# Performance work log

Hardware: AMD Instinct MI355X
Metric: run time of the kernel (lower is better)

The kernel has to match this reference:

```python
import jax, jax.numpy as jnp
import numpy as np

B, S, D = 2, 2048, 2048
H, NOPE, ROPE, V, C = 16, 128, 64, 128, 512
QK = NOPE + ROPE


def setup_inputs() -> dict:
    key = jax.random.key(0)
    ks = jax.random.split(key, 5)
    x = jax.random.normal(ks[0], (B, S, D), jnp.float32)
    # RoPE angle tables (seqlen, rope_dim/2)
    inv = 1.0 / (10000.0 ** (np.arange(0, ROPE, 2, dtype=np.float64) / ROPE))
    ang = np.arange(S, dtype=np.float64)[:, None] * inv[None, :]
    freqs_cos = jnp.asarray(np.cos(ang), jnp.float32)
    freqs_sin = jnp.asarray(np.sin(ang), jnp.float32)
    wq = jax.random.normal(ks[1], (H * QK, D), jnp.float32) * 0.02
    wkv_a = jax.random.normal(ks[2], (C + ROPE, D), jnp.float32) * 0.02
    wkv_b = jax.random.normal(ks[3], (H * (NOPE + V), C), jnp.float32) * 0.02
    wo = jax.random.normal(ks[4], (D, H * V), jnp.float32) * 0.02
    return {"x": x, "freqs_cos": freqs_cos, "freqs_sin": freqs_sin,
            "wq": wq, "wkv_a": wkv_a, "wkv_b": wkv_b, "wo": wo}


def _rope(t, cos, sin):
    # t: (b, s, h, r) with interleaved (real, imag) pairs, matching
    # torch.view_as_complex on reshape(..., r//2, 2)
    tr, ti = t[..., 0::2], t[..., 1::2]
    cos = cos[None, :, None, :]
    sin = sin[None, :, None, :]
    orr = tr * cos - ti * sin
    oii = tr * sin + ti * cos
    return jnp.stack([orr, oii], axis=-1).reshape(t.shape)


def _rmsnorm(t, eps=1e-6):
    return t * jax.lax.rsqrt(jnp.mean(t * t, axis=-1, keepdims=True) + eps)


def reference(x, freqs_cos, freqs_sin, wq, wkv_a, wkv_b, wo):
    # q projection (q_lora_rank == 0 -> direct)
    q = (x @ wq.T).reshape(B, S, H, QK)
    q_nope, q_pe = q[..., :NOPE], q[..., NOPE:]
    q_pe = _rope(q_pe, freqs_cos, freqs_sin)
    # latent KV compression
    kv = x @ wkv_a.T  # (b, s, C + ROPE)
    c, k_pe = kv[..., :C], kv[..., C:]
    k_pe = _rope(k_pe[:, :, None, :], freqs_cos, freqs_sin)[:, :, 0, :]  # (b, s, ROPE)
    c = _rmsnorm(c)  # cached latent (b, s, C)
    # weight absorption: wkv_b -> (H, NOPE+V, C)
    wb = wkv_b.reshape(H, NOPE + V, C)
    w_nope, w_v = wb[:, :NOPE, :], wb[:, NOPE:, :]
    q_abs = jnp.einsum('bshd,hdc->bshc', q_nope, w_nope)  # absorbed query
    scale = QK ** -0.5
    scores = (jnp.einsum('bshc,btc->bhst', q_abs, c)
              + jnp.einsum('bshr,btr->bhst', q_pe, k_pe)) * scale
    attn = jax.nn.softmax(scores, axis=-1)
    out_c = jnp.einsum('bhst,btc->bshc', attn, c)
    out = jnp.einsum('bshc,hvc->bshv', out_c, w_v)  # (b, s, h, V)
    return out.reshape(B, S, H * V) @ wo.T
```

## Files before the change

### kernel.cpp

```cpp
#include <hip/hip_runtime.h>

#define B_ 2
#define S_ 2048
#define D_ 2048
#define H_ 16
#define NOPE_ 128
#define ROPE_ 64
#define V_ 128
#define C_ 512
#define QK_ 192
#define CR_ 576
#define BS_ 4096

typedef unsigned short ushort_t;
typedef unsigned int uint_t;
typedef __attribute__((ext_vector_type(8))) short bf16x8;
typedef __attribute__((ext_vector_type(4))) float f32x4;

#define GLD16(gp, lp) __builtin_amdgcn_global_load_lds( \
    (const __attribute__((address_space(1))) void*)(gp), \
    (__attribute__((address_space(3))) void*)(lp), 16, 0, 0)

__device__ __forceinline__ float us2f(ushort_t u) {
    unsigned int x = ((unsigned int)u) << 16;
    return __uint_as_float(x);
}
__device__ __forceinline__ ushort_t f2us(float f) {
    unsigned int x = __float_as_uint(f);
    unsigned int r = (x + 0x7fffu + ((x >> 16) & 1u)) >> 16;
    return (ushort_t)r;
}

__global__ __launch_bounds__(256) void conv_all_k(
    const float* __restrict__ x,    ushort_t* __restrict__ xb,
    const float* __restrict__ wq,   ushort_t* __restrict__ wqb,
    const float* __restrict__ wo,   ushort_t* __restrict__ wob,
    const float* __restrict__ wkva, ushort_t* __restrict__ wkvab,
    const float* __restrict__ wkvb, ushort_t* __restrict__ wvb)
{
    int bid = blockIdx.x;
    if (bid < 8192) {
        long long i = ((long long)bid * 256 + threadIdx.x) * 4;
        float4 v = *reinterpret_cast<const float4*>(x + i);
        ushort4 o; o.x = f2us(v.x); o.y = f2us(v.y); o.z = f2us(v.z); o.w = f2us(v.w);
        *reinterpret_cast<ushort4*>(xb + i) = o;
    } else if (bid < 14336) {
        long long i = ((long long)(bid - 8192) * 256 + threadIdx.x) * 4;
        float4 v = *reinterpret_cast<const float4*>(wq + i);
        ushort4 o; o.x = f2us(v.x); o.y = f2us(v.y); o.z = f2us(v.z); o.w = f2us(v.w);
        *reinterpret_cast<ushort4*>(wqb + i) = o;
    } else if (bid < 18432) {
        long long i = ((long long)(bid - 14336) * 256 + threadIdx.x) * 4;
        float4 v = *reinterpret_cast<const float4*>(wo + i);
        ushort4 o; o.x = f2us(v.x); o.y = f2us(v.y); o.z = f2us(v.z); o.w = f2us(v.w);
        *reinterpret_cast<ushort4*>(wob + i) = o;
    } else if (bid < 19712) {
        long long i = ((long long)(bid - 18432) * 256 + threadIdx.x) * 4;
        int row = (int)(i >> 11);
        ushort4 o;
        if (row < 576) {
            float4 v = *reinterpret_cast<const float4*>(wkva + i);
            o.x = f2us(v.x); o.y = f2us(v.y); o.z = f2us(v.z); o.w = f2us(v.w);
        } else { o.x = o.y = o.z = o.w = 0; }
        *reinterpret_cast<ushort4*>(wkvab + i) = o;
    } else {
        long long i = ((long long)(bid - 19712) * 256 + threadIdx.x) * 4;
        int h = (int)(i >> 16);
        int rem = (int)(i & 65535);
        float4 v = *reinterpret_cast<const float4*>(wkvb + (long long)h * 131072 + 65536 + rem);
        ushort4 o; o.x = f2us(v.x); o.y = f2us(v.y); o.z = f2us(v.z); o.w = f2us(v.w);
        *reinterpret_cast<ushort4*>(wvb + i) = o;
    }
}

__global__ __launch_bounds__(256) void conv_wnt_k(
    const float* __restrict__ wkvb, ushort_t* __restrict__ wnT)
{
    __shared__ float st[32][33];
    int h = blockIdx.z;
    int d0 = blockIdx.x * 32, c0 = blockIdx.y * 32;
    int t = threadIdx.x;
    int dl = t >> 3, c4 = (t & 7) * 4;
    float4 v = *reinterpret_cast<const float4*>(
        wkvb + (long long)h * 131072 + (d0 + dl) * 512 + c0 + c4);
    st[dl][c4] = v.x; st[dl][c4+1] = v.y; st[dl][c4+2] = v.z; st[dl][c4+3] = v.w;
    __syncthreads();
    int cl = t >> 3, d4 = (t & 7) * 4;
    ushort4 o;
    o.x = f2us(st[d4][cl]);   o.y = f2us(st[d4+1][cl]);
    o.z = f2us(st[d4+2][cl]); o.w = f2us(st[d4+3][cl]);
    *reinterpret_cast<ushort4*>(wnT + (long long)h * 65536 + (c0 + cl) * 128 + d0 + d4) = o;
}

template <typename TC, bool NGUARD>
__global__ __launch_bounds__(256) void gemm_mfma_k(
    const ushort_t* __restrict__ A, int lda, long long strideAz,
    const ushort_t* __restrict__ Bm, int ldb, long long strideBz,
    TC* __restrict__ Cm, int ldc, long long strideCz,
    int K, int N_real)
{
    __shared__ ushort_t sA[128 * 32];
    __shared__ ushort_t sB[128 * 32];
    const int tid = threadIdx.x;
    const int w = tid >> 6, ln = tid & 63;
    const int g = ln >> 4, r16 = ln & 15;
    const int wr = w >> 1, wc = w & 1;
    const int z = blockIdx.z;
    A  += (long long)z * strideAz;
    Bm += (long long)z * strideBz;
    Cm += (long long)z * strideCz;
    const long long m0 = (long long)blockIdx.y * 128;
    const long long n0 = (long long)blockIdx.x * 128;

    const int r0 = tid >> 2, kc8 = (tid & 3) * 8;
    const ushort_t* a0 = A + (m0 + r0) * lda + kc8;
    const ushort_t* a1 = A + (m0 + 64 + r0) * lda + kc8;
    const ushort_t* b0 = Bm + (n0 + r0) * ldb + kc8;
    const ushort_t* b1 = Bm + (n0 + 64 + r0) * ldb + kc8;
    ushort_t* sA0 = sA + w * 512;
    ushort_t* sA1 = sA + 2048 + w * 512;
    ushort_t* sB0 = sB + w * 512;
    ushort_t* sB1 = sB + 2048 + w * 512;

    const f32x4 zero4 = {0.f, 0.f, 0.f, 0.f};
    f32x4 acc[4][4];
    #pragma unroll
    for (int i = 0; i < 4; ++i)
        #pragma unroll
        for (int j = 0; j < 4; ++j) acc[i][j] = zero4;

    for (int k0 = 0; k0 < K; k0 += 32) {
        GLD16(a0 + k0, sA0);
        GLD16(a1 + k0, sA1);
        GLD16(b0 + k0, sB0);
        GLD16(b1 + k0, sB1);
        __syncthreads();
        bf16x8 af[4], bfr[4];
        #pragma unroll
        for (int i = 0; i < 4; ++i)
            af[i] = *reinterpret_cast<const bf16x8*>(&sA[(64 * wr + 16 * i + r16) * 32 + 8 * g]);
        #pragma unroll
        for (int j = 0; j < 4; ++j)
            bfr[j] = *reinterpret_cast<const bf16x8*>(&sB[(64 * wc + 16 * j + r16) * 32 + 8 * g]);
        __builtin_amdgcn_s_setprio(1);
        #pragma unroll
        for (int i = 0; i < 4; ++i)
            #pragma unroll
            for (int j = 0; j < 4; ++j)
                acc[i][j] = __builtin_amdgcn_mfma_f32_16x16x32_bf16(af[i], bfr[j], acc[i][j], 0, 0, 0);
        __builtin_amdgcn_s_setprio(0);
        __syncthreads();
    }
    #pragma unroll
    for (int i = 0; i < 4; ++i) {
        #pragma unroll
        for (int j = 0; j < 4; ++j) {
            int nn = (int)n0 + 64 * wc + 16 * j + r16;
            if (NGUARD && nn >= N_real) continue;
            #pragma unroll
            for (int r = 0; r < 4; ++r) {
                long long row = m0 + 64 * wr + 16 * i + 4 * g + r;
                float v = acc[i][j][r];
                if constexpr (sizeof(TC) == 2) Cm[row * ldc + nn] = (TC)f2us(v);
                else                           Cm[row * ldc + nn] = (TC)v;
            }
        }
    }
}

__global__ __launch_bounds__(256) void rope_q_k(
    const ushort_t* __restrict__ qb, ushort_t* __restrict__ qcat,
    const float* __restrict__ fc, const float* __restrict__ fs)
{
    int id = blockIdx.x * 256 + threadIdx.x;
    int i  = id & 31;
    int h  = (id >> 5) & 15;
    int bs = id >> 9;
    int s  = bs & (S_ - 1);
    float c  = fc[s * 32 + i];
    float sn = fs[s * 32 + i];
    uint_t w2 = *reinterpret_cast<const uint_t*>(
        qb + (long long)bs * 3072 + h * QK_ + NOPE_ + 2 * i);
    float tr = us2f((ushort_t)(w2 & 0xffffu));
    float ti = us2f((ushort_t)(w2 >> 16));
    float orr = tr * c - ti * sn;
    float oii = tr * sn + ti * c;
    uint_t wrd = (uint_t)f2us(orr) | ((uint_t)f2us(oii) << 16);
    ((uint_t*)qcat)[((long long)h * BS_ + bs) * 288 + 256 + i] = wrd;
}

__global__ __launch_bounds__(256) void kvpost_k(
    const float* __restrict__ kv, ushort_t* __restrict__ kvb16,
    const float* __restrict__ fc, const float* __restrict__ fs)
{
    int bs = blockIdx.x;
    const float* row = kv + (long long)bs * CR_;
    ushort_t* orow = kvb16 + (long long)bs * CR_;
    int tid = threadIdx.x;
    float v0 = row[tid], v1 = row[tid + 256];
    float ss = v0 * v0 + v1 * v1;
    #pragma unroll
    for (int m = 1; m < 64; m <<= 1) ss += __shfl_xor(ss, m, 64);
    __shared__ float red[4];
    if ((tid & 63) == 0) red[tid >> 6] = ss;
    __syncthreads();
    float tot = red[0] + red[1] + red[2] + red[3];
    float r = rsqrtf(tot * (1.0f / (float)C_) + 1e-6f);
    orow[tid] = f2us(v0 * r);
    orow[tid + 256] = f2us(v1 * r);
    if (tid < 32) {
        int s = bs & (S_ - 1);
        float c  = fc[s * 32 + tid];
        float sn = fs[s * 32 + tid];
        float tr = row[C_ + 2 * tid], ti = row[C_ + 2 * tid + 1];
        orow[C_ + 2 * tid]     = f2us(tr * c - ti * sn);
        orow[C_ + 2 * tid + 1] = f2us(tr * sn + ti * c);
    }
}

__global__ __launch_bounds__(256) void vtrans_k(
    const ushort_t* __restrict__ kvb16, ushort_t* __restrict__ vT16)
{
    __shared__ ushort_t st[32][36];
    int b = blockIdx.z;
    int s0 = blockIdx.x * 32, c0 = blockIdx.y * 32;
    int t = threadIdx.x;
    int sl = t >> 3, c4 = (t & 7) * 4;
    ushort4 v = *reinterpret_cast<const ushort4*>(
        kvb16 + ((long long)(b * S_ + s0 + sl)) * CR_ + c0 + c4);
    st[sl][c4] = v.x; st[sl][c4+1] = v.y; st[sl][c4+2] = v.z; st[sl][c4+3] = v.w;
    __syncthreads();
    int cl = t >> 3, s4 = (t & 7) * 4;
    ushort4 o;
    o.x = st[s4][cl]; o.y = st[s4+1][cl]; o.z = st[s4+2][cl]; o.w = st[s4+3][cl];
    *reinterpret_cast<ushort4*>(
        vT16 + ((long long)b * 512 + c0 + cl) * 2048 + s0 + s4) = o;
}

__global__ __launch_bounds__(512, 2) void attn_mfma_k(
    const ushort_t* __restrict__ qcat,
    const ushort_t* __restrict__ kvb16,
    const ushort_t* __restrict__ vT16,
    ushort_t* __restrict__ outc)
{
    __shared__ ushort_t sKV[2 * 32 * 576];
    __shared__ ushort_t sVT[2 * 512 * 32];

    const int tid = threadIdx.x;
    const int w   = tid >> 6;
    const int ln  = tid & 63;
    const int g   = ln >> 4;
    const int r16 = ln & 15;
    const int bh = blockIdx.y;
    const int b = bh >> 4, h = bh & 15;
    const int s0 = blockIdx.x * 128;

    int kvoff[4], kvoff4 = 0;
    #pragma unroll
    for (int i = 0; i < 4; ++i) {
        int p = i * 512 + tid;
        int row = p / 72, cs = p - row * 72;
        kvoff[i] = row * 576 + ((cs & ~7) | ((cs ^ row) & 7)) * 8;
    }
    if (w < 4) {
        int p = 2048 + tid;
        int row = p / 72, cs = p - row * 72;
        kvoff4 = row * 576 + ((cs & ~7) | ((cs ^ row) & 7)) * 8;
    }
    int vtoff[4];
    #pragma unroll
    for (int i = 0; i < 4; ++i) {
        int p = i * 512 + tid;
        int rp = p >> 3, sw = p & 7;
        int lg = sw ^ (rp & 7);
        vtoff[i] = (2 * rp + (lg >> 2)) * 2048 + (lg & 3) * 8;
    }

    bf16x8 qfrag[18];
    {
        const ushort_t* qp = qcat
            + ((long long)h * BS_ + (long long)b * S_ + (s0 + 16 * w + r16)) * 576 + 8 * g;
        #pragma unroll
        for (int kt = 0; kt < 18; ++kt)
            qfrag[kt] = *reinterpret_cast<const bf16x8*>(qp + 32 * kt);
    }

    const f32x4 zero4 = {0.f, 0.f, 0.f, 0.f};
    f32x4 acc[32];
    #pragma unroll
    for (int i = 0; i < 32; ++i) acc[i] = zero4;

    float m_run = -1e30f, l_run = 0.0f;
    const float scale = 0.0721687836487032f;

    const ushort_t* kvsrc = kvb16 + (long long)b * S_ * 576;
    const ushort_t* vtsrc = vT16 + (long long)b * 512 * 2048;
    char* skvb = (char*)sKV;
    char* svtb = (char*)sVT;

#define STAGE_TILE(T0, DB) do { \
        const ushort_t* kvt_ = kvsrc + (long long)(T0) * 576; \
        const ushort_t* vtt_ = vtsrc + (T0); \
        _Pragma("unroll") \
        for (int i_ = 0; i_ < 4; ++i_) \
            GLD16(kvt_ + kvoff[i_], skvb + (DB) * 36864 + i_ * 8192 + w * 1024); \
        if (w < 4) GLD16(kvt_ + kvoff4, skvb + (DB) * 36864 + 32768 + w * 1024); \
        _Pragma("unroll") \
        for (int i_ = 0; i_ < 4; ++i_) \
            GLD16(vtt_ + vtoff[i_], svtb + (DB) * 32768 + i_ * 8192 + w * 1024); \
    } while (0)

    STAGE_TILE(0, 0);

    for (int t = 0; t < 64; ++t) {
        const int cur = t & 1;
        asm volatile("s_waitcnt vmcnt(0)" ::: "memory");
        __builtin_amdgcn_s_barrier();
        __builtin_amdgcn_sched_barrier(0);
        if (t < 63) STAGE_TILE((t + 1) * 32, cur ^ 1);

        const int kvb = cur * 18432;
        f32x4 d0a = zero4, d0b = zero4, d1a = zero4, d1b = zero4;
        __builtin_amdgcn_s_setprio(1);
        #pragma unroll
        for (int kt = 0; kt < 9; ++kt) {
            int ch = kt * 4 + g;
            int chs = (ch & ~7) | ((ch ^ r16) & 7);
            bf16x8 a0 = *reinterpret_cast<const bf16x8*>(&sKV[kvb + r16 * 576 + chs * 8]);
            bf16x8 a1 = *reinterpret_cast<const bf16x8*>(&sKV[kvb + (16 + r16) * 576 + chs * 8]);
            d0a = __builtin_amdgcn_mfma_f32_16x16x32_bf16(a0, qfrag[kt], d0a, 0, 0, 0);
            d1a = __builtin_amdgcn_mfma_f32_16x16x32_bf16(a1, qfrag[kt], d1a, 0, 0, 0);
        }
        #pragma unroll
        for (int kt = 9; kt < 18; ++kt) {
            int ch = kt * 4 + g;
            int chs = (ch & ~7) | ((ch ^ r16) & 7);
            bf16x8 a0 = *reinterpret_cast<const bf16x8*>(&sKV[kvb + r16 * 576 + chs * 8]);
            bf16x8 a1 = *reinterpret_cast<const bf16x8*>(&sKV[kvb + (16 + r16) * 576 + chs * 8]);
            d0b = __builtin_amdgcn_mfma_f32_16x16x32_bf16(a0, qfrag[kt], d0b, 0, 0, 0);
            d1b = __builtin_amdgcn_mfma_f32_16x16x32_bf16(a1, qfrag[kt], d1b, 0, 0, 0);
        }
        __builtin_amdgcn_s_setprio(0);
        f32x4 d0 = d0a + d0b, d1 = d1a + d1b;

        float p[8];
        #pragma unroll
        for (int i = 0; i < 4; ++i) { p[i] = d0[i] * scale; p[4 + i] = d1[i] * scale; }
        float mt = p[0];
        #pragma unroll
        for (int i = 1; i < 8; ++i) mt = fmaxf(mt, p[i]);
        mt = fmaxf(mt, __shfl_xor(mt, 16, 64));
        mt = fmaxf(mt, __shfl_xor(mt, 32, 64));
        bool anyneed = __any(mt > m_run + 8.0f);
        float m_new = anyneed ? fmaxf(m_run, mt) : m_run;
        float fac = anyneed ? __expf(m_run - m_new) : 1.0f;
        m_run = m_new;
        float lt = 0.f;
        #pragma unroll
        for (int i = 0; i < 8; ++i) { p[i] = __expf(p[i] - m_new); lt += p[i]; }
        lt += __shfl_xor(lt, 16, 64);
        lt += __shfl_xor(lt, 32, 64);
        l_run = l_run * fac + lt;

        uint_t w0, w1, w2, w3;
        asm("v_cvt_pk_bf16_f32 %0, %1, %2" : "=v"(w0) : "v"(p[0]), "v"(p[1]));
        asm("v_cvt_pk_bf16_f32 %0, %1, %2" : "=v"(w1) : "v"(p[2]), "v"(p[3]));
        asm("v_cvt_pk_bf16_f32 %0, %1, %2" : "=v"(w2) : "v"(p[4]), "v"(p[5]));
        asm("v_cvt_pk_bf16_f32 %0, %1, %2" : "=v"(w3) : "v"(p[6]), "v"(p[7]));
        uint_t xa = (uint_t)__shfl_xor((int)((g & 1) ? w0 : w2), 16, 64);
        uint_t xb = (uint_t)__shfl_xor((int)((g & 1) ? w1 : w3), 16, 64);
        uint_t ya = (uint_t)__shfl_xor((int)((g >> 1) ? w0 : w2), 32, 64);
        uint_t yb = (uint_t)__shfl_xor((int)((g >> 1) ? w1 : w3), 32, 64);
        uint_t za = (uint_t)__shfl_xor((int)((g == 1) ? w2 : w0), 48, 64);
        uint_t zb = (uint_t)__shfl_xor((int)((g == 1) ? w3 : w1), 48, 64);
        uint_t pw[4];
        if      (g == 0) { pw[0] = w0; pw[1] = w1; pw[2] = xa; pw[3] = xb; }
        else if (g == 1) { pw[0] = za; pw[1] = zb; pw[2] = ya; pw[3] = yb; }
        else if (g == 2) { pw[0] = ya; pw[1] = yb; pw[2] = za; pw[3] = zb; }
        else             { pw[0] = xa; pw[1] = xb; pw[2] = w2; pw[3] = w3; }
        bf16x8 pB = *reinterpret_cast<bf16x8*>(pw);

        if (anyneed) {
            #pragma unroll
            for (int ct = 0; ct < 32; ++ct) {
                acc[ct][0] *= fac; acc[ct][1] *= fac;
                acc[ct][2] *= fac; acc[ct][3] *= fac;
            }
        }
        const int vtb = cur * 16384;
        __builtin_amdgcn_s_setprio(1);
        #pragma unroll
        for (int ct = 0; ct < 32; ++ct) {
            int c = 16 * ct + r16;
            int sw = ((c & 1) * 4 + g) ^ ((c >> 1) & 7);
            bf16x8 aV = *reinterpret_cast<const bf16x8*>(&sVT[vtb + (c >> 1) * 64 + sw * 8]);
            acc[ct] = __builtin_amdgcn_mfma_f32_16x16x32_bf16(aV, pB, acc[ct], 0, 0, 0);
        }
        __builtin_amdgcn_s_setprio(0);
    }
#undef STAGE_TILE

    float inv = 1.0f / l_run;
    long long row = (long long)b * S_ + s0 + 16 * w + r16;
    ushort_t* obase = outc + row * 8192 + h * 512;
    #pragma unroll
    for (int ct = 0; ct < 32; ++ct) {
        int cg = 16 * ct + 4 * g;
        ushort4 o;
        o.x = f2us(acc[ct][0] * inv);
        o.y = f2us(acc[ct][1] * inv);
        o.z = f2us(acc[ct][2] * inv);
        o.w = f2us(acc[ct][3] * inv);
        *reinterpret_cast<ushort4*>(obase + cg) = o;
    }
}

extern "C" void kernel_launch(void* const* d_in, const int* in_sizes, int n_in,
                              void* d_out, int out_size, void* d_ws, size_t ws_size,
                              hipStream_t stream)
{
    if (ws_size < 221773824ULL) return;
    const float* x    = (const float*)d_in[0];
    const float* fc   = (const float*)d_in[1];
    const float* fs   = (const float*)d_in[2];
    const float* wq   = (const float*)d_in[3];
    const float* wkva = (const float*)d_in[4];
    const float* wkvb = (const float*)d_in[5];
    const float* wo   = (const float*)d_in[6];
    float* out = (float*)d_out;

    char* ws = (char*)d_ws;
    ushort_t* qcat  = (ushort_t*)(ws);
    ushort_t* outc  = (ushort_t*)(ws + 75497472);
    ushort_t* qb16  = (ushort_t*)(ws + 142606336);
    ushort_t* xb    = (ushort_t*)(ws + 167772160);
    ushort_t* aoutb = (ushort_t*)(ws + 167772160);
    ushort_t* wqb   = (ushort_t*)(ws + 184549376);
    ushort_t* kvb16 = (ushort_t*)(ws + 184549376);
    ushort_t* vT16  = (ushort_t*)(ws + 189267968);
    float*    kvbuf = (float*)(ws + 197132288);
    ushort_t* wob   = (ushort_t*)(ws + 206569472);
    ushort_t* wkvab = (ushort_t*)(ws + 214958080);
    ushort_t* wnTb  = (ushort_t*)(ws + 217579520);
    ushort_t* wvb   = (ushort_t*)(ws + 219676672);

    conv_all_k<<<dim3(20736), 256, 0, stream>>>(
        x, xb, wq, wqb, wo, wob, wkva, wkvab, wkvb, wvb);
    conv_wnt_k<<<dim3(4, 16, 16), 256, 0, stream>>>(wkvb, wnTb);
    gemm_mfma_k<ushort_t, false><<<dim3(24, 32, 1), 256, 0, stream>>>(
        xb, D_, 0, wqb, D_, 0, qb16, 3072, 0, D_, 3072);
    gemm_mfma_k<float, true><<<dim3(5, 32, 1), 256, 0, stream>>>(
        xb, D_, 0, wkvab, D_, 0, kvbuf, CR_, 0, D_, CR_);
    rope_q_k<<<dim3(BS_ * H_ * 32 / 256), 256, 0, stream>>>(qb16, qcat, fc, fs);
    kvpost_k<<<dim3(BS_), 256, 0, stream>>>(kvbuf, kvb16, fc, fs);
    vtrans_k<<<dim3(S_ / 32, C_ / 32, B_), 256, 0, stream>>>(kvb16, vT16);
    gemm_mfma_k<ushort_t, false><<<dim3(4, 32, 16), 256, 0, stream>>>(
        qb16, 3072, 192, wnTb, 128, 65536, qcat, 576, (long long)BS_ * 576, NOPE_, 512);
    attn_mfma_k<<<dim3(S_ / 128, B_ * H_), 512, 0, stream>>>(qcat, kvb16, vT16, outc);
    gemm_mfma_k<ushort_t, false><<<dim3(1, 32, 16), 256, 0, stream>>>(
        outc, 8192, 512, wvb, 512, 65536, aoutb, 2048, 128, C_, 128);
    gemm_mfma_k<float, false><<<dim3(16, 32, 1), 256, 0, stream>>>(
        aoutb, 2048, 0, wob, 2048, 0, out, D_, 0, 2048, 2048);
}
```

Measured before the change: 702.2 us.

## Halve attention KV tile to 16 keys and use 16x16x16 MFMA for PV

Shrinks the per-iteration key tile from 32 to 16 rows, halving LDS staging buffers and doubling the loop count. The P·V product switches to a 16x16x16 bf16 MFMA driven through inline asm, which removes the cross-lane shuffle repacking of probabilities, and the V transpose swizzle in LDS is redone to match. The intent is to cut LDS footprint and shuffle overhead in exchange for twice as many barriers, softmax reductions and rescale checks, and half the MFMA K-depth per instruction. Manual s_nop padding is added around the inline-asm MFMAs for hazard safety.

```diff
diff --git a/kernel.cpp b/kernel.cpp
--- a/kernel.cpp
+++ b/kernel.cpp
@@ -15,6 +15,7 @@
 typedef unsigned short ushort_t;
 typedef unsigned int uint_t;
 typedef __attribute__((ext_vector_type(8))) short bf16x8;
+typedef __attribute__((ext_vector_type(4))) short bf16x4;
 typedef __attribute__((ext_vector_type(4))) float f32x4;
 
 #define GLD16(gp, lp) __builtin_amdgcn_global_load_lds( \
@@ -243,8 +244,8 @@
     const ushort_t* __restrict__ vT16,
     ushort_t* __restrict__ outc)
 {
-    __shared__ ushort_t sKV[2 * 32 * 576];
-    __shared__ ushort_t sVT[2 * 512 * 32];
+    __shared__ ushort_t sKV[2 * 16 * 576];
+    __shared__ ushort_t sVT[2 * 512 * 16];
 
     const int tid = threadIdx.x;
     const int w   = tid >> 6;
@@ -255,25 +256,25 @@
     const int b = bh >> 4, h = bh & 15;
     const int s0 = blockIdx.x * 128;
 
-    int kvoff[4], kvoff4 = 0;
-    #pragma unroll
-    for (int i = 0; i < 4; ++i) {
+    int kvoff[2], kvoff2 = 0;
+    #pragma unroll
+    for (int i = 0; i < 2; ++i) {
         int p = i * 512 + tid;
         int row = p / 72, cs = p - row * 72;
         kvoff[i] = row * 576 + ((cs & ~7) | ((cs ^ row) & 7)) * 8;
     }
-    if (w < 4) {
-        int p = 2048 + tid;
+    if (tid < 128) {
+        int p = 1024 + tid;
         int row = p / 72, cs = p - row * 72;
-        kvoff4 = row * 576 + ((cs & ~7) | ((cs ^ row) & 7)) * 8;
-    }
-    int vtoff[4];
-    #pragma unroll
-    for (int i = 0; i < 4; ++i) {
+        kvoff2 = row * 576 + ((cs & ~7) | ((cs ^ row) & 7)) * 8;
+    }
+    int vtoff[2];
+    #pragma unroll
+    for (int i = 0; i < 2; ++i) {
         int p = i * 512 + tid;
-        int rp = p >> 3, sw = p & 7;
-        int lg = sw ^ (rp & 7);
-        vtoff[i] = (2 * rp + (lg >> 2)) * 2048 + (lg & 3) * 8;
+        int c = p >> 1;
+        int lg = (p & 1) ^ ((c >> 2) & 1);
+        vtoff[i] = c * 2048 + lg * 8;
     }
 
     bf16x8 qfrag[18];
@@ -301,54 +302,46 @@
 #define STAGE_TILE(T0, DB) do { \
         const ushort_t* kvt_ = kvsrc + (long long)(T0) * 576; \
         const ushort_t* vtt_ = vtsrc + (T0); \
-        _Pragma("unroll") \
-        for (int i_ = 0; i_ < 4; ++i_) \
-            GLD16(kvt_ + kvoff[i_], skvb + (DB) * 36864 + i_ * 8192 + w * 1024); \
-        if (w < 4) GLD16(kvt_ + kvoff4, skvb + (DB) * 36864 + 32768 + w * 1024); \
-        _Pragma("unroll") \
-        for (int i_ = 0; i_ < 4; ++i_) \
-            GLD16(vtt_ + vtoff[i_], svtb + (DB) * 32768 + i_ * 8192 + w * 1024); \
+        GLD16(kvt_ + kvoff[0], skvb + (DB) * 18432 + w * 1024); \
+        GLD16(kvt_ + kvoff[1], skvb + (DB) * 18432 + 8192 + w * 1024); \
+        if (tid < 128) GLD16(kvt_ + kvoff2, skvb + (DB) * 18432 + 16384 + w * 1024); \
+        GLD16(vtt_ + vtoff[0], svtb + (DB) * 16384 + w * 1024); \
+        GLD16(vtt_ + vtoff[1], svtb + (DB) * 16384 + 8192 + w * 1024); \
     } while (0)
 
     STAGE_TILE(0, 0);
 
-    for (int t = 0; t < 64; ++t) {
+    for (int t = 0; t < 128; ++t) {
         const int cur = t & 1;
         asm volatile("s_waitcnt vmcnt(0)" ::: "memory");
         __builtin_amdgcn_s_barrier();
         __builtin_amdgcn_sched_barrier(0);
-        if (t < 63) STAGE_TILE((t + 1) * 32, cur ^ 1);
-
-        const int kvb = cur * 18432;
-        f32x4 d0a = zero4, d0b = zero4, d1a = zero4, d1b = zero4;
+        if (t < 127) STAGE_TILE((t + 1) * 16, cur ^ 1);
+
+        const int kvb = cur * 9216;
+        f32x4 d0a = zero4, d0b = zero4;
         __builtin_amdgcn_s_setprio(1);
         #pragma unroll
         for (int kt = 0; kt < 9; ++kt) {
             int ch = kt * 4 + g;
             int chs = (ch & ~7) | ((ch ^ r16) & 7);
             bf16x8 a0 = *reinterpret_cast<const bf16x8*>(&sKV[kvb + r16 * 576 + chs * 8]);
-            bf16x8 a1 = *reinterpret_cast<const bf16x8*>(&sKV[kvb + (16 + r16) * 576 + chs * 8]);
             d0a = __builtin_amdgcn_mfma_f32_16x16x32_bf16(a0, qfrag[kt], d0a, 0, 0, 0);
-            d1a = __builtin_amdgcn_mfma_f32_16x16x32_bf16(a1, qfrag[kt], d1a, 0, 0, 0);
         }
         #pragma unroll
         for (int kt = 9; kt < 18; ++kt) {
             int ch = kt * 4 + g;
             int chs = (ch & ~7) | ((ch ^ r16) & 7);
             bf16x8 a0 = *reinterpret_cast<const bf16x8*>(&sKV[kvb + r16 * 576 + chs * 8]);
-            bf16x8 a1 = *reinterpret_cast<const bf16x8*>(&sKV[kvb + (16 + r16) * 576 + chs * 8]);
             d0b = __builtin_amdgcn_mfma_f32_16x16x32_bf16(a0, qfrag[kt], d0b, 0, 0, 0);
-            d1b = __builtin_amdgcn_mfma_f32_16x16x32_bf16(a1, qfrag[kt], d1b, 0, 0, 0);
         }
         __builtin_amdgcn_s_setprio(0);
-        f32x4 d0 = d0a + d0b, d1 = d1a + d1b;
-
-        float p[8];
-        #pragma unroll
-        for (int i = 0; i < 4; ++i) { p[i] = d0[i] * scale; p[4 + i] = d1[i] * scale; }
-        float mt = p[0];
-        #pragma unroll
-        for (int i = 1; i < 8; ++i) mt = fmaxf(mt, p[i]);
+        f32x4 d0 = d0a + d0b;
+
+        float p[4];
+        #pragma unroll
+        for (int i = 0; i < 4; ++i) p[i] = d0[i] * scale;
+        float mt = fmaxf(fmaxf(p[0], p[1]), fmaxf(p[2], p[3]));
         mt = fmaxf(mt, __shfl_xor(mt, 16, 64));
         mt = fmaxf(mt, __shfl_xor(mt, 32, 64));
         bool anyneed = __any(mt > m_run + 8.0f);
@@ -357,28 +350,15 @@
         m_run = m_new;
         float lt = 0.f;
         #pragma unroll
-        for (int i = 0; i < 8; ++i) { p[i] = __expf(p[i] - m_new); lt += p[i]; }
+        for (int i = 0; i < 4; ++i) { p[i] = __expf(p[i] - m_new); lt += p[i]; }
         lt += __shfl_xor(lt, 16, 64);
         lt += __shfl_xor(lt, 32, 64);
         l_run = l_run * fac + lt;
 
-        uint_t w0, w1, w2, w3;
-        asm("v_cvt_pk_bf16_f32 %0, %1, %2" : "=v"(w0) : "v"(p[0]), "v"(p[1]));
-        asm("v_cvt_pk_bf16_f32 %0, %1, %2" : "=v"(w1) : "v"(p[2]), "v"(p[3]));
-        asm("v_cvt_pk_bf16_f32 %0, %1, %2" : "=v"(w2) : "v"(p[4]), "v"(p[5]));
-        asm("v_cvt_pk_bf16_f32 %0, %1, %2" : "=v"(w3) : "v"(p[6]), "v"(p[7]));
-        uint_t xa = (uint_t)__shfl_xor((int)((g & 1) ? w0 : w2), 16, 64);
-        uint_t xb = (uint_t)__shfl_xor((int)((g & 1) ? w1 : w3), 16, 64);
-        uint_t ya = (uint_t)__shfl_xor((int)((g >> 1) ? w0 : w2), 32, 64);
-        uint_t yb = (uint_t)__shfl_xor((int)((g >> 1) ? w1 : w3), 32, 64);
-        uint_t za = (uint_t)__shfl_xor((int)((g == 1) ? w2 : w0), 48, 64);
-        uint_t zb = (uint_t)__shfl_xor((int)((g == 1) ? w3 : w1), 48, 64);
-        uint_t pw[4];
-        if      (g == 0) { pw[0] = w0; pw[1] = w1; pw[2] = xa; pw[3] = xb; }
-        else if (g == 1) { pw[0] = za; pw[1] = zb; pw[2] = ya; pw[3] = yb; }
-        else if (g == 2) { pw[0] = ya; pw[1] = yb; pw[2] = za; pw[3] = zb; }
-        else             { pw[0] = xa; pw[1] = xb; pw[2] = w2; pw[3] = w3; }
-        bf16x8 pB = *reinterpret_cast<bf16x8*>(pw);
+        uint_t pw[2];
+        asm("v_cvt_pk_bf16_f32 %0, %1, %2" : "=v"(pw[0]) : "v"(p[0]), "v"(p[1]));
+        asm("v_cvt_pk_bf16_f32 %0, %1, %2" : "=v"(pw[1]) : "v"(p[2]), "v"(p[3]));
+        bf16x4 pB = *reinterpret_cast<bf16x4*>(pw);
 
         if (anyneed) {
             #pragma unroll
@@ -387,14 +367,17 @@
                 acc[ct][2] *= fac; acc[ct][3] *= fac;
             }
         }
-        const int vtb = cur * 16384;
+        asm volatile("s_nop 4" :::);
+
+        const int vtb = cur * 8192;
         __builtin_amdgcn_s_setprio(1);
         #pragma unroll
         for (int ct = 0; ct < 32; ++ct) {
             int c = 16 * ct + r16;
-            int sw = ((c & 1) * 4 + g) ^ ((c >> 1) & 7);
-            bf16x8 aV = *reinterpret_cast<const bf16x8*>(&sVT[vtb + (c >> 1) * 64 + sw * 8]);
-            acc[ct] = __builtin_amdgcn_mfma_f32_16x16x32_bf16(aV, pB, acc[ct], 0, 0, 0);
+            int elem = c * 16 + (((g >> 1) ^ ((c >> 2) & 1)) << 3) + ((g & 1) << 2);
+            bf16x4 aV = *reinterpret_cast<const bf16x4*>(&sVT[vtb + elem]);
+            asm("v_mfma_f32_16x16x16_bf16 %0, %1, %2, %0"
+                : "+v"(acc[ct]) : "v"(aV), "v"(pB));
         }
         __builtin_amdgcn_s_setprio(0);
     }
@@ -403,6 +386,8 @@
     float inv = 1.0f / l_run;
     long long row = (long long)b * S_ + s0 + 16 * w + r16;
     ushort_t* obase = outc + row * 8192 + h * 512;
+    asm volatile("s_nop 7" :::);
+    asm volatile("s_nop 7" :::);
     #pragma unroll
     for (int ct = 0; ct < 32; ++ct) {
         int cg = 16 * ct + 4 * g;
```

Result: slower. 876.4 us (+24.8%).
